# Kernel tuning notes

Hardware: AMD Instinct MI355X
Metric: run time of the kernel (lower is better)

The kernel has to match this reference:

```python
import jax, jax.numpy as jnp
import numpy as np

H = 256  # rnn hidden size

def _rnn_dir(x, wih, whh, bih, bhh):
    # x: [B,T,D] -> outputs [B,T,H]; h_t = tanh(x_t Wih^T + bih + h_{t-1} Whh^T + bhh)
    xproj = jnp.einsum('btd,hd->bth', x, wih) + bih + bhh  # precompute input projection
    def step(h, xp):
        h = jnp.tanh(xp + h @ whh.T)
        return h, h
    h0 = jnp.zeros((x.shape[0], whh.shape[0]), x.dtype)
    _, ys = jax.lax.scan(step, h0, jnp.swapaxes(xproj, 0, 1))
    return jnp.swapaxes(ys, 0, 1)

def _birnn(x, wif, whf, bif, bhf, wib, whb, bib, bhb):
    fwd = _rnn_dir(x, wif, whf, bif, bhf)
    bwd = _rnn_dir(x[:, ::-1, :], wib, whb, bib, bhb)[:, ::-1, :]
    return jnp.concatenate([fwd, bwd], axis=-1)

def setup_inputs() -> dict:
    key = jax.random.key(0)
    ks = jax.random.split(key, 24)
    B, T, V, E = 64, 512, 131072, 128
    s = 0.05
    emb = jax.random.normal(ks[0], (V, E), jnp.float32) * s
    emb = emb.at[0].set(0.0)  # padding_idx=0
    def W(k, shp):
        return jax.random.normal(k, shp, jnp.float32) * s
    inp = {
        'x': jax.random.randint(ks[1], (B, T), 0, V),
        'emb': emb,
        'r1_wif': W(ks[2], (H, E)), 'r1_whf': W(ks[3], (H, H)),
        'r1_bif': W(ks[4], (H,)), 'r1_bhf': W(ks[5], (H,)),
        'r1_wib': W(ks[6], (H, E)), 'r1_whb': W(ks[7], (H, H)),
        'r1_bib': W(ks[8], (H,)), 'r1_bhb': W(ks[9], (H,)),
        'r2_wif': W(ks[10], (H, 2 * H)), 'r2_whf': W(ks[11], (H, H)),
        'r2_bif': W(ks[12], (H,)), 'r2_bhf': W(ks[13], (H,)),
        'r2_wib': W(ks[14], (H, 2 * H)), 'r2_whb': W(ks[15], (H, H)),
        'r2_bib': W(ks[16], (H,)), 'r2_bhb': W(ks[17], (H,)),
        'ln_g': jnp.ones((1024,), jnp.float32),
        'ln_b': jnp.zeros((1024,), jnp.float32),
        'w1': W(ks[18], (512, 1024)), 'b1': W(ks[19], (512,)),
        'w2': W(ks[20], (256, 512)), 'b2': W(ks[21], (256,)),
    }
    return inp

def reference(x, emb, r1_wif, r1_whf, r1_bif, r1_bhf, r1_wib, r1_whb, r1_bib, r1_bhb,
              r2_wif, r2_whf, r2_bif, r2_bhf, r2_wib, r2_whb, r2_bib, r2_bhb,
              ln_g, ln_b, w1, b1, w2, b2):
    e = emb[x]  # [B,T,128]
    o1 = _birnn(e, r1_wif, r1_whf, r1_bif, r1_bhf, r1_wib, r1_whb, r1_bib, r1_bhb)  # [B,T,512]
    o2 = _birnn(o1, r2_wif, r2_whf, r2_bif, r2_bhf, r2_wib, r2_whb, r2_bib, r2_bhb)  # [B,T,512]
    last = o2[:, -1, :]
    mean = jnp.mean(o2, axis=1)
    h = jnp.concatenate([last, mean], axis=1)  # [B,1024]
    mu = jnp.mean(h, axis=-1, keepdims=True)
    var = jnp.mean(jnp.square(h - mu), axis=-1, keepdims=True)
    h = (h - mu) * jax.lax.rsqrt(var + 1e-5) * ln_g + ln_b
    h = jax.nn.relu(h @ w1.T + b1)
    return h @ w2.T + b2
```

## Files before the change

### kernel.cpp

```cpp
#include <hip/hip_runtime.h>
#include <stdint.h>

typedef unsigned short u16;
typedef unsigned int   u32;
typedef __attribute__((ext_vector_type(8))) short short8;
typedef __attribute__((ext_vector_type(4))) float f32x4;

#define T_LEN 512
#define HID   256

__device__ __forceinline__ float bflo(u32 u){ union{u32 i; float f;} v; v.i = u << 16; return v.f; }
__device__ __forceinline__ float bfhi(u32 u){ union{u32 i; float f;} v; v.i = u & 0xffff0000u; return v.f; }
__device__ __forceinline__ float b2f(u16 s){ union{u32 i; float f;} v; v.i = ((u32)s) << 16; return v.f; }
__device__ __forceinline__ u16 f2b(float f){
  union{float f; u32 i;} v; v.f = f;
  u32 r = v.i + 0x7fffu + ((v.i >> 16) & 1u);
  return (u16)(r >> 16);
}
__device__ __forceinline__ u32 pk2(float a, float b){ return (u32)f2b(a) | ((u32)f2b(b) << 16); }
__device__ __forceinline__ float tanh_fast(float x){
  float ax = fabsf(x);
  float e  = __expf(-2.f * ax);
  float t  = (1.f - e) * __builtin_amdgcn_rcpf(1.f + e);
  return copysignf(t, x);
}
__device__ __forceinline__ bool flag_bf16(const u32* f){ return (f[0] & 0xFFFFu) == 0x3F80u; }

#define NT 22
struct ConvArgs {
  const void* src[NT];
  u32 off[NT];
  u32 total;
  const u32* flagsrc;
};

__global__ __launch_bounds__(256)
void convert_params(ConvArgs a, u16* __restrict__ dst)
{
  const bool bf = flag_bf16(a.flagsrc);
  const u32 stride = gridDim.x * blockDim.x;
  for (u32 g = blockIdx.x * blockDim.x + threadIdx.x; g < a.total; g += stride) {
    int t = 0;
    #pragma unroll
    for (int i = 1; i < NT; ++i) t += (g >= a.off[i]);
    u32 local = g - a.off[t];
    dst[g] = bf ? ((const u16*)a.src[t])[local]
                : f2b(((const float*)a.src[t])[local]);
  }
}

template<int K, int SRC>
__global__ __launch_bounds__(256, 2)
void wgemm(const void* Bsrc, const int* __restrict__ gidx,
           const u16* __restrict__ Wf, const u16* __restrict__ Wb,
           const u16* __restrict__ bif, const u16* __restrict__ bhf,
           const u16* __restrict__ bib, const u16* __restrict__ bhb,
           u16* outT, const u32* flagsrc)
{
  __shared__ __align__(16) u16 lds[64 * K];
  const int tid  = threadIdx.x;
  const int row0 = blockIdx.x * 64;
  const int bb   = row0 >> 9;
  const int t0   = row0 & 511;
  const int bt   = bb >> 4, nb = bb & 15;
  constexpr int CPR = K / 8;

  bool abf = true;
  if (SRC == 0) abf = flag_bf16(flagsrc);

  for (int i = tid; i < 64 * CPR; i += 256) {
    int r = i / CPR, c = i % CPR;
    uint4 v;
    if (SRC == 0) {
      long rb = (long)gidx[row0 + r] * K;
      if (abf) {
        v = *(const uint4*)((const u16*)Bsrc + rb + c * 8);
      } else {
        const float* af = (const float*)Bsrc;
        float4 lo = *(const float4*)(af + rb + c * 8);
        float4 hi = *(const float4*)(af + rb + c * 8 + 4);
        v.x = pk2(lo.x, lo.y); v.y = pk2(lo.z, lo.w);
        v.z = pk2(hi.x, hi.y); v.w = pk2(hi.z, hi.w);
      }
    } else {
      int k = c * 8, d = k >> 8;
      size_t e = (size_t)(d * 4 + bt) * 2097152 + (size_t)(t0 + r) * 4096
               + (size_t)nb * 256 + (k & 255);
      v = *(const uint4*)((const u16*)Bsrc + e);
    }
    *(uint4*)&lds[r * K + ((c ^ (r & 7)) * 8)] = v;
  }
  __syncthreads();

  const int w = tid >> 6, lane = tid & 63, n16 = lane & 15, quad = lane >> 4;
  const int d = w >> 1;
  const u16* W  = d ? Wb : Wf;
  const u16* bi = d ? bib : bif;
  const u16* bh = d ? bhb : bhf;
  const int mbase = (w & 1) * 128;

  f32x4 acc[8][4];
  #pragma unroll
  for (int i = 0; i < 8; ++i)
    #pragma unroll
    for (int j = 0; j < 4; ++j) acc[i][j] = (f32x4){0.f, 0.f, 0.f, 0.f};

  #pragma unroll
  for (int kk = 0; kk < K / 32; ++kk) {
    short8 bfr[4];
    #pragma unroll
    for (int j = 0; j < 4; ++j) {
      int r = j * 16 + n16;
      int c = (kk * 4 + quad) ^ (r & 7);
      bfr[j] = *(const short8*)&lds[r * K + c * 8];
    }
    #pragma unroll
    for (int i = 0; i < 8; ++i) {
      short8 afr = *(const short8*)(W + (size_t)(mbase + i * 16 + n16) * K + kk * 32 + quad * 8);
      #pragma unroll
      for (int j = 0; j < 4; ++j)
        acc[i][j] = __builtin_amdgcn_mfma_f32_16x16x32_bf16(afr, bfr[j], acc[i][j], 0, 0, 0);
    }
  }

  #pragma unroll
  for (int i = 0; i < 8; ++i) {
    int mrow0 = mbase + i * 16 + quad * 4;
    uint2 biv = *(const uint2*)(bi + mrow0);
    uint2 bhv = *(const uint2*)(bh + mrow0);
    float bias0 = b2f(biv.x & 0xffff) + b2f(bhv.x & 0xffff);
    float bias1 = b2f(biv.x >> 16)    + b2f(bhv.x >> 16);
    float bias2 = b2f(biv.y & 0xffff) + b2f(bhv.y & 0xffff);
    float bias3 = b2f(biv.y >> 16)    + b2f(bhv.y >> 16);
    #pragma unroll
    for (int j = 0; j < 4; ++j) {
      int t = t0 + j * 16 + n16;
      uint2 pv;
      pv.x = pk2(acc[i][j][0] + bias0, acc[i][j][1] + bias1);
      pv.y = pk2(acc[i][j][2] + bias2, acc[i][j][3] + bias3);
      size_t e = (size_t)(d * 4 + bt) * 2097152 + (size_t)t * 4096
               + (size_t)nb * 256 + mrow0;
      *(uint2*)(outT + e) = pv;
    }
  }
}

template<int MODE>
__device__ __forceinline__ void scan_step(
    int s, int dir, int n16, int quad, int m0,
    const u16 (&hrd)[16][264], u16 (&hwr)[16][264],
    uint2& pf,
    const u16* xptr, u16* optr,
    const short8 (&wa)[8], f32x4& sum, float* lastb, int lbase)
{
  const int t = dir ? (511 - s) : s;
  const uint2 xv = pf;
  {
    int s2 = (s + 2 < 512) ? s + 2 : 511;
    int t2 = dir ? (511 - s2) : s2;
    pf = *(const uint2*)(xptr + (size_t)t2 * 4096);
  }

  short8 hb[8];
  #pragma unroll
  for (int kk = 0; kk < 8; ++kk)
    hb[kk] = *(const short8*)&hrd[n16][kk * 32 + quad * 8];

  f32x4 acc0 = (f32x4){0.f, 0.f, 0.f, 0.f};
  f32x4 acc1 = (f32x4){0.f, 0.f, 0.f, 0.f};
  #pragma unroll
  for (int kk = 0; kk < 4; ++kk) {
    acc0 = __builtin_amdgcn_mfma_f32_16x16x32_bf16(wa[kk],     hb[kk],     acc0, 0, 0, 0);
    acc1 = __builtin_amdgcn_mfma_f32_16x16x32_bf16(wa[kk + 4], hb[kk + 4], acc1, 0, 0, 0);
  }

  float h0 = tanh_fast(acc0[0] + acc1[0] + b2f(xv.x & 0xffff));
  float h1 = tanh_fast(acc0[1] + acc1[1] + b2f(xv.x >> 16));
  float h2 = tanh_fast(acc0[2] + acc1[2] + b2f(xv.y & 0xffff));
  float h3 = tanh_fast(acc0[3] + acc1[3] + b2f(xv.y >> 16));
  uint2 hv; hv.x = pk2(h0, h1); hv.y = pk2(h2, h3);
  *(uint2*)&hwr[n16][m0] = hv;

  if (MODE == 0) {
    *(uint2*)(optr + (size_t)t * 4096) = hv;
  } else {
    sum += (f32x4){h0, h1, h2, h3};
    if (s == (dir ? 0 : 511))
      *(float4*)&lastb[(size_t)lbase] = (float4){h0, h1, h2, h3};
  }
  __syncthreads();
}

template<int MODE>
__global__ __launch_bounds__(1024)
void rnn_scan(const u16* xpT,
              const u16* __restrict__ whhF, const u16* __restrict__ whhB,
              u16* o1T, float* __restrict__ lastb, float* __restrict__ sumb)
{
  __shared__ __align__(16) u16 hl[2][16][264];
  const int tid = threadIdx.x, w = tid >> 6, lane = tid & 63;
  const int n16 = lane & 15, quad = lane >> 4;
  const int dir = blockIdx.x >> 2, bt = blockIdx.x & 3;
  const u16* whh = dir ? whhB : whhF;
  const int m0 = w * 16 + quad * 4;

  short8 wa[8];
  #pragma unroll
  for (int kk = 0; kk < 8; ++kk)
    wa[kk] = *(const short8*)(whh + (size_t)(w * 16 + n16) * 256 + kk * 32 + quad * 8);

  for (int i = tid; i < 16 * 264; i += 1024) ((u16*)hl[0])[i] = 0;

  const size_t blkbase = (size_t)(dir * 4 + bt) * 2097152;
  const u16* xptr = xpT + blkbase + (size_t)n16 * 256 + m0;
  u16*       optr = o1T + blkbase + (size_t)n16 * 256 + m0;
  const int lbase = (dir * 64 + bt * 16 + n16) * 256 + m0;

  uint2 pf0, pf1;
  {
    int ta = dir ? 511 : 0, tb = dir ? 510 : 1;
    pf0 = *(const uint2*)(xptr + (size_t)ta * 4096);
    pf1 = *(const uint2*)(xptr + (size_t)tb * 4096);
  }
  f32x4 sum = (f32x4){0.f, 0.f, 0.f, 0.f};
  __syncthreads();

  for (int s = 0; s < 512; s += 2) {
    scan_step<MODE>(s,     dir, n16, quad, m0, hl[0], hl[1], pf0, xptr, optr, wa, sum, lastb, lbase);
    scan_step<MODE>(s + 1, dir, n16, quad, m0, hl[1], hl[0], pf1, xptr, optr, wa, sum, lastb, lbase);
  }

  if (MODE == 1)
    *(float4*)&sumb[(size_t)lbase] = (float4){sum[0], sum[1], sum[2], sum[3]};
}

__device__ __forceinline__ float dot8(uint4 q, const float* hp){
  return bflo(q.x)*hp[0] + bfhi(q.x)*hp[1] + bflo(q.y)*hp[2] + bfhi(q.y)*hp[3]
       + bflo(q.z)*hp[4] + bfhi(q.z)*hp[5] + bflo(q.w)*hp[6] + bfhi(q.w)*hp[7];
}

__global__ __launch_bounds__(256)
void head_kernel(const float* __restrict__ lastb, const float* __restrict__ sumb,
                 const u16* __restrict__ g, const u16* __restrict__ be,
                 const u16* __restrict__ w1, const u16* __restrict__ b1,
                 const u16* __restrict__ w2, const u16* __restrict__ b2,
                 void* outv, const u32* flagsrc)
{
  __shared__ __align__(16) float hv[1024];
  __shared__ __align__(16) float act[512];
  __shared__ float red[8];
  const int tid = threadIdx.x;
  const int b   = blockIdx.x;
  const bool bf = flag_bf16(flagsrc);

  float v0 = lastb[b * 256 + tid];
  float v1 = lastb[(64 + b) * 256 + tid];
  float v2 = sumb[b * 256 + tid] * (1.f / 512.f);
  float v3 = sumb[(64 + b) * 256 + tid] * (1.f / 512.f);
  hv[tid] = v0; hv[256 + tid] = v1; hv[512 + tid] = v2; hv[768 + tid] = v3;

  float s  = v0 + v1 + v2 + v3;
  float ss = v0*v0 + v1*v1 + v2*v2 + v3*v3;
  #pragma unroll
  for (int off = 32; off; off >>= 1) {
    s  += __shfl_down(s, off);
    ss += __shfl_down(ss, off);
  }
  if ((tid & 63) == 0) { red[tid >> 6] = s; red[4 + (tid >> 6)] = ss; }
  __syncthreads();
  float S  = red[0] + red[1] + red[2] + red[3];
  float SS = red[4] + red[5] + red[6] + red[7];
  float mu   = S * (1.f / 1024.f);
  float var  = SS * (1.f / 1024.f) - mu * mu;
  float rstd = rsqrtf(var + 1e-5f);

  #pragma unroll
  for (int i = 0; i < 4; ++i) {
    int idx = i * 256 + tid;
    hv[idx] = (hv[idx] - mu) * rstd * b2f(g[idx]) + b2f(be[idx]);
  }
  __syncthreads();

  #pragma unroll
  for (int jj = 0; jj < 2; ++jj) {
    int j = jj * 256 + tid;
    const uint4* wr = (const uint4*)(w1 + (long)j * 1024);
    float a = 0.f;
    for (int c = 0; c < 128; ++c) a += dot8(wr[c], &hv[c * 8]);
    a += b2f(b1[j]);
    act[j] = a > 0.f ? a : 0.f;
  }
  __syncthreads();

  const uint4* wr2 = (const uint4*)(w2 + (long)tid * 512);
  float a = 0.f;
  for (int c = 0; c < 64; ++c) a += dot8(wr2[c], &act[c * 8]);
  a += b2f(b2[tid]);

  if (bf) {
    ((u16*)outv)[b * 256 + tid] = f2b(a);
  } else {
    union { u32 i; float f; } u; u.i = ((u32)f2b(a)) << 16;
    ((float*)outv)[b * 256 + tid] = u.f;
  }
}

extern "C" void kernel_launch(void* const* d_in, const int* in_sizes, int n_in,
                              void* d_out, int out_size, void* d_ws, size_t ws_size,
                              hipStream_t stream)
{
  const int* x    = (const int*)d_in[0];
  const u32* flag = (const u32*)d_in[18];

  static const int sizes[NT] = {
    32768, 65536, 256, 256, 32768, 65536, 256, 256,
    131072, 65536, 256, 256, 131072, 65536, 256, 256,
    1024, 1024, 524288, 512, 131072, 256
  };
  ConvArgs ca;
  u32 off = 0;
  for (int i = 0; i < NT; ++i) {
    ca.src[i] = d_in[2 + i];
    ca.off[i] = off;
    off += (u32)sizes[i];
  }
  ca.total = off;
  ca.flagsrc = flag;

  char* ws = (char*)d_ws;
  u16*   buf    = (u16*)ws;
  u16*   pm     = (u16*)(ws + 33554432);
  float* lastb  = (float*)(ws + 36054528);
  float* sumb   = (float*)(ws + 36185600);

  const u16* p_r1wif = pm + 0;
  const u16* p_r1whf = pm + 32768;
  const u16* p_r1bif = pm + 98304;
  const u16* p_r1bhf = pm + 98560;
  const u16* p_r1wib = pm + 98816;
  const u16* p_r1whb = pm + 131584;
  const u16* p_r1bib = pm + 197120;
  const u16* p_r1bhb = pm + 197376;
  const u16* p_r2wif = pm + 197632;
  const u16* p_r2whf = pm + 328704;
  const u16* p_r2bif = pm + 394240;
  const u16* p_r2bhf = pm + 394496;
  const u16* p_r2wib = pm + 394752;
  const u16* p_r2whb = pm + 525824;
  const u16* p_r2bib = pm + 591360;
  const u16* p_r2bhb = pm + 591616;
  const u16* p_lng   = pm + 591872;
  const u16* p_lnb   = pm + 592896;
  const u16* p_w1    = pm + 593920;
  const u16* p_b1    = pm + 1118208;
  const u16* p_w2    = pm + 1118720;
  const u16* p_b2    = pm + 1249792;

  convert_params<<<1024, 256, 0, stream>>>(ca, pm);

  wgemm<128, 0><<<512, 256, 0, stream>>>(d_in[1], x,
      p_r1wif, p_r1wib, p_r1bif, p_r1bhf, p_r1bib, p_r1bhb, buf, flag);
  rnn_scan<0><<<8, 1024, 0, stream>>>(buf, p_r1whf, p_r1whb, buf, nullptr, nullptr);
  wgemm<512, 1><<<512, 256, 0, stream>>>(buf, nullptr,
      p_r2wif, p_r2wib, p_r2bif, p_r2bhf, p_r2bib, p_r2bhb, buf, flag);
  rnn_scan<1><<<8, 1024, 0, stream>>>(buf, p_r2whf, p_r2whb, nullptr, lastb, sumb);
  head_kernel<<<64, 256, 0, stream>>>(lastb, sumb, p_lng, p_lnb, p_w1, p_b1, p_w2, p_b2,
      d_out, flag);
}
```

Before: 1.058 ms.

## Halve RNN scan block size with two row tiles per wave and Pade tanh

```diff
diff --git a/kernel.cpp b/kernel.cpp
--- a/kernel.cpp
+++ b/kernel.cpp
@@ -1,10 +1,12 @@
 #include <hip/hip_runtime.h>
+#include <hip/hip_bf16.h>
 #include <stdint.h>
 
 typedef unsigned short u16;
 typedef unsigned int   u32;
 typedef __attribute__((ext_vector_type(8))) short short8;
 typedef __attribute__((ext_vector_type(4))) float f32x4;
+typedef __attribute__((ext_vector_type(2))) float f32x2v;
 
 #define T_LEN 512
 #define HID   256
@@ -18,11 +20,21 @@
   return (u16)(r >> 16);
 }
 __device__ __forceinline__ u32 pk2(float a, float b){ return (u32)f2b(a) | ((u32)f2b(b) << 16); }
-__device__ __forceinline__ float tanh_fast(float x){
-  float ax = fabsf(x);
-  float e  = __expf(-2.f * ax);
-  float t  = (1.f - e) * __builtin_amdgcn_rcpf(1.f + e);
-  return copysignf(t, x);
+__device__ __forceinline__ u32 pkb(float a, float b){
+#if __has_builtin(__builtin_amdgcn_cvt_pk_bf16_f32)
+  typedef __attribute__((ext_vector_type(2))) __bf16 bf16x2;
+  bf16x2 h = __builtin_amdgcn_cvt_pk_bf16_f32(a, b);
+  union { bf16x2 h; u32 u; } v; v.h = h; return v.u;
+#else
+  return pk2(a, b);
+#endif
+}
+__device__ __forceinline__ float tanh_pade(float x){
+  float t = x * x;
+  float num = x * fmaf(t, 105.f + t, 945.f);
+  float den = fmaf(t, fmaf(15.f, t, 420.f), 945.f);
+  float r = num * __builtin_amdgcn_rcpf(den);
+  return fminf(fmaxf(r, -1.f), 1.f);
 }
 __device__ __forceinline__ bool flag_bf16(const u32* f){ return (f[0] & 0xFFFFu) == 0x3F80u; }
 
@@ -147,18 +159,20 @@
 
 template<int MODE>
 __device__ __forceinline__ void scan_step(
-    int s, int dir, int n16, int quad, int m0,
+    int s, int dir, int n16, int quad, int m0, int m1,
     const u16 (&hrd)[16][264], u16 (&hwr)[16][264],
-    uint2& pf,
-    const u16* xptr, u16* optr,
-    const short8 (&wa)[8], f32x4& sum, float* lastb, int lbase)
+    uint2& pfa, uint2& pfb,
+    const u16* xptr0, const u16* xptr1, u16* optr0, u16* optr1,
+    const short8 (&wa)[2][8], f32x4& sum0, f32x4& sum1,
+    float* lastb, int lbase)
 {
   const int t = dir ? (511 - s) : s;
-  const uint2 xv = pf;
+  const uint2 xv0 = pfa, xv1 = pfb;
   {
     int s2 = (s + 2 < 512) ? s + 2 : 511;
     int t2 = dir ? (511 - s2) : s2;
-    pf = *(const uint2*)(xptr + (size_t)t2 * 4096);
+    pfa = *(const uint2*)(xptr0 + (size_t)t2 * 4096);
+    pfb = *(const uint2*)(xptr1 + (size_t)t2 * 4096);
   }
 
   short8 hb[8];
@@ -166,33 +180,44 @@
   for (int kk = 0; kk < 8; ++kk)
     hb[kk] = *(const short8*)&hrd[n16][kk * 32 + quad * 8];
 
-  f32x4 acc0 = (f32x4){0.f, 0.f, 0.f, 0.f};
-  f32x4 acc1 = (f32x4){0.f, 0.f, 0.f, 0.f};
+  f32x4 a00 = (f32x4){0.f,0.f,0.f,0.f}, a01 = a00, a10 = a00, a11 = a00;
   #pragma unroll
   for (int kk = 0; kk < 4; ++kk) {
-    acc0 = __builtin_amdgcn_mfma_f32_16x16x32_bf16(wa[kk],     hb[kk],     acc0, 0, 0, 0);
-    acc1 = __builtin_amdgcn_mfma_f32_16x16x32_bf16(wa[kk + 4], hb[kk + 4], acc1, 0, 0, 0);
-  }
-
-  float h0 = tanh_fast(acc0[0] + acc1[0] + b2f(xv.x & 0xffff));
-  float h1 = tanh_fast(acc0[1] + acc1[1] + b2f(xv.x >> 16));
-  float h2 = tanh_fast(acc0[2] + acc1[2] + b2f(xv.y & 0xffff));
-  float h3 = tanh_fast(acc0[3] + acc1[3] + b2f(xv.y >> 16));
-  uint2 hv; hv.x = pk2(h0, h1); hv.y = pk2(h2, h3);
+    a00 = __builtin_amdgcn_mfma_f32_16x16x32_bf16(wa[0][kk],     hb[kk],     a00, 0, 0, 0);
+    a01 = __builtin_amdgcn_mfma_f32_16x16x32_bf16(wa[0][kk + 4], hb[kk + 4], a01, 0, 0, 0);
+    a10 = __builtin_amdgcn_mfma_f32_16x16x32_bf16(wa[1][kk],     hb[kk],     a10, 0, 0, 0);
+    a11 = __builtin_amdgcn_mfma_f32_16x16x32_bf16(wa[1][kk + 4], hb[kk + 4], a11, 0, 0, 0);
+  }
+
+  float h0 = tanh_pade(a00[0] + a01[0] + bflo(xv0.x));
+  float h1 = tanh_pade(a00[1] + a01[1] + bfhi(xv0.x));
+  float h2 = tanh_pade(a00[2] + a01[2] + bflo(xv0.y));
+  float h3 = tanh_pade(a00[3] + a01[3] + bfhi(xv0.y));
+  float g0 = tanh_pade(a10[0] + a11[0] + bflo(xv1.x));
+  float g1 = tanh_pade(a10[1] + a11[1] + bfhi(xv1.x));
+  float g2 = tanh_pade(a10[2] + a11[2] + bflo(xv1.y));
+  float g3 = tanh_pade(a10[3] + a11[3] + bfhi(xv1.y));
+  uint2 hv; hv.x = pkb(h0, h1); hv.y = pkb(h2, h3);
+  uint2 gv; gv.x = pkb(g0, g1); gv.y = pkb(g2, g3);
   *(uint2*)&hwr[n16][m0] = hv;
+  *(uint2*)&hwr[n16][m1] = gv;
 
   if (MODE == 0) {
-    *(uint2*)(optr + (size_t)t * 4096) = hv;
+    *(uint2*)(optr0 + (size_t)t * 4096) = hv;
+    *(uint2*)(optr1 + (size_t)t * 4096) = gv;
   } else {
-    sum += (f32x4){h0, h1, h2, h3};
-    if (s == (dir ? 0 : 511))
-      *(float4*)&lastb[(size_t)lbase] = (float4){h0, h1, h2, h3};
+    sum0 += (f32x4){h0, h1, h2, h3};
+    sum1 += (f32x4){g0, g1, g2, g3};
+    if (s == (dir ? 0 : 511)) {
+      *(float4*)&lastb[(size_t)lbase]      = (float4){h0, h1, h2, h3};
+      *(float4*)&lastb[(size_t)lbase + 16] = (float4){g0, g1, g2, g3};
+    }
   }
   __syncthreads();
 }
 
 template<int MODE>
-__global__ __launch_bounds__(1024)
+__global__ __launch_bounds__(512)
 void rnn_scan(const u16* xpT,
               const u16* __restrict__ whhF, const u16* __restrict__ whhB,
               u16* o1T, float* __restrict__ lastb, float* __restrict__ sumb)
@@ -202,36 +227,48 @@
   const int n16 = lane & 15, quad = lane >> 4;
   const int dir = blockIdx.x >> 2, bt = blockIdx.x & 3;
   const u16* whh = dir ? whhB : whhF;
-  const int m0 = w * 16 + quad * 4;
-
-  short8 wa[8];
-  #pragma unroll
-  for (int kk = 0; kk < 8; ++kk)
-    wa[kk] = *(const short8*)(whh + (size_t)(w * 16 + n16) * 256 + kk * 32 + quad * 8);
-
-  for (int i = tid; i < 16 * 264; i += 1024) ((u16*)hl[0])[i] = 0;
+  const int m0 = (2 * w) * 16 + quad * 4;
+  const int m1 = m0 + 16;
+
+  short8 wa[2][8];
+  #pragma unroll
+  for (int ti = 0; ti < 2; ++ti)
+    #pragma unroll
+    for (int kk = 0; kk < 8; ++kk)
+      wa[ti][kk] = *(const short8*)(whh + (size_t)((2 * w + ti) * 16 + n16) * 256
+                                    + kk * 32 + quad * 8);
+
+  for (int i = tid; i < 16 * 264; i += 512) ((u16*)hl[0])[i] = 0;
 
   const size_t blkbase = (size_t)(dir * 4 + bt) * 2097152;
-  const u16* xptr = xpT + blkbase + (size_t)n16 * 256 + m0;
-  u16*       optr = o1T + blkbase + (size_t)n16 * 256 + m0;
+  const u16* xptr0 = xpT + blkbase + (size_t)n16 * 256 + m0;
+  const u16* xptr1 = xptr0 + 16;
+  u16* optr0 = o1T + blkbase + (size_t)n16 * 256 + m0;
+  u16* optr1 = optr0 + 16;
   const int lbase = (dir * 64 + bt * 16 + n16) * 256 + m0;
 
-  uint2 pf0, pf1;
+  uint2 pf0a, pf0b, pf1a, pf1b;
   {
     int ta = dir ? 511 : 0, tb = dir ? 510 : 1;
-    pf0 = *(const uint2*)(xptr + (size_t)ta * 4096);
-    pf1 = *(const uint2*)(xptr + (size_t)tb * 4096);
-  }
-  f32x4 sum = (f32x4){0.f, 0.f, 0.f, 0.f};
+    pf0a = *(const uint2*)(xptr0 + (size_t)ta * 4096);
+    pf0b = *(const uint2*)(xptr1 + (size_t)ta * 4096);
+    pf1a = *(const uint2*)(xptr0 + (size_t)tb * 4096);
+    pf1b = *(const uint2*)(xptr1 + (size_t)tb * 4096);
+  }
+  f32x4 sum0 = (f32x4){0.f,0.f,0.f,0.f}, sum1 = sum0;
   __syncthreads();
 
   for (int s = 0; s < 512; s += 2) {
-    scan_step<MODE>(s,     dir, n16, quad, m0, hl[0], hl[1], pf0, xptr, optr, wa, sum, lastb, lbase);
-    scan_step<MODE>(s + 1, dir, n16, quad, m0, hl[1], hl[0], pf1, xptr, optr, wa, sum, lastb, lbase);
-  }
-
-  if (MODE == 1)
-    *(float4*)&sumb[(size_t)lbase] = (float4){sum[0], sum[1], sum[2], sum[3]};
+    scan_step<MODE>(s,     dir, n16, quad, m0, m1, hl[0], hl[1], pf0a, pf0b,
+                    xptr0, xptr1, optr0, optr1, wa, sum0, sum1, lastb, lbase);
+    scan_step<MODE>(s + 1, dir, n16, quad, m0, m1, hl[1], hl[0], pf1a, pf1b,
+                    xptr0, xptr1, optr0, optr1, wa, sum0, sum1, lastb, lbase);
+  }
+
+  if (MODE == 1) {
+    *(float4*)&sumb[(size_t)lbase]      = (float4){sum0[0], sum0[1], sum0[2], sum0[3]};
+    *(float4*)&sumb[(size_t)lbase + 16] = (float4){sum1[0], sum1[1], sum1[2], sum1[3]};
+  }
 }
 
 __device__ __forceinline__ float dot8(uint4 q, const float* hp){
@@ -360,10 +397,10 @@
 
   wgemm<128, 0><<<512, 256, 0, stream>>>(d_in[1], x,
       p_r1wif, p_r1wib, p_r1bif, p_r1bhf, p_r1bib, p_r1bhb, buf, flag);
-  rnn_scan<0><<<8, 1024, 0, stream>>>(buf, p_r1whf, p_r1whb, buf, nullptr, nullptr);
+  rnn_scan<0><<<8, 512, 0, stream>>>(buf, p_r1whf, p_r1whb, buf, nullptr, nullptr);
   wgemm<512, 1><<<512, 256, 0, stream>>>(buf, nullptr,
       p_r2wif, p_r2wib, p_r2bif, p_r2bhf, p_r2bib, p_r2bhb, buf, flag);
-  rnn_scan<1><<<8, 1024, 0, stream>>>(buf, p_r2whf, p_r2whb, nullptr, lastb, sumb);
+  rnn_scan<1><<<8, 512, 0, stream>>>(buf, p_r2whf, p_r2whb, nullptr, lastb, sumb);
   head_kernel<<<64, 256, 0, stream>>>(lastb, sumb, p_lng, p_lnb, p_w1, p_b1, p_w2, p_b2,
       d_out, flag);
 }
```

New measurement: 1.116 ms. 1.06x slower.
